# Performance work log

Measured on AMD Instinct MI355X. Metric: run time of the kernel, lower is better.

The kernel has to match this reference:

```python
import jax, jax.numpy as jnp
import numpy as np

B, NQ, NKV, D, H, HD = 8, 1024, 2048, 1024, 16, 64  # inner_dim = H*HD = 1024


def setup_inputs() -> dict:
    key = jax.random.key(0)
    ks = jax.random.split(key, 10)
    s = 0.02
    return {
        "latent": jax.random.normal(ks[0], (B, NQ, D), jnp.float32),
        "data": jax.random.normal(ks[1], (B, NKV, D), jnp.float32),
        "wq": jax.random.normal(ks[2], (D, H * HD), jnp.float32) * s,
        "bq": jax.random.normal(ks[3], (H * HD,), jnp.float32) * s,
        "wk": jax.random.normal(ks[4], (D, H * HD), jnp.float32) * s,
        "bk": jax.random.normal(ks[5], (H * HD,), jnp.float32) * s,
        "wv": jax.random.normal(ks[6], (D, H * HD), jnp.float32) * s,
        "bv": jax.random.normal(ks[7], (H * HD,), jnp.float32) * s,
        "wo": jax.random.normal(ks[8], (H * HD, D), jnp.float32) * s,
        "bo": jax.random.normal(ks[9], (D,), jnp.float32) * s,
    }


def reference(latent, data, wq, bq, wk, bk, wv, bv, wo, bo):
    scale = HD ** -0.5
    # projections: [b, n, H*HD] -> [b, h, n, d]
    def split_heads(t):
        b, n, _ = t.shape
        return t.reshape(b, n, H, HD).transpose(0, 2, 1, 3)

    q = split_heads(latent @ wq + bq)   # [b, h, nq, d]
    k = split_heads(data @ wk + bk)     # [b, h, nkv, d]
    v = split_heads(data @ wv + bv)     # [b, h, nkv, d]

    scores = jnp.einsum("bhid,bhjd->bhij", q, k) * scale  # [b, h, nq, nkv]
    att = jax.nn.softmax(scores, axis=-1)                  # dropout p=0 (eval)
    out = jnp.einsum("bhij,bhjd->bhid", att, v)            # [b, h, nq, d]
    out = out.transpose(0, 2, 1, 3).reshape(B, NQ, H * HD)
    return out @ wo + bo
```

## Files before the change

### kernel.cpp

```cpp
#include <hip/hip_runtime.h>
#include <hip/hip_bf16.h>
#include <math.h>


using short8  = __attribute__((ext_vector_type(8))) short;
using f32x4   = __attribute__((ext_vector_type(4))) float;
using uint4v  = __attribute__((ext_vector_type(4))) unsigned int;

__device__ __forceinline__ ushort f2bf(float f) {
    unsigned u = __builtin_bit_cast(unsigned, f);
    u = (u + 0x7FFFu + ((u >> 16) & 1u)) >> 16;
    return (ushort)u;
}
__device__ __forceinline__ unsigned pack_bf2(float lo, float hi) {
    unsigned ulo = __builtin_bit_cast(unsigned, lo) + 0x8000u;
    unsigned uhi = __builtin_bit_cast(unsigned, hi) + 0x8000u;
    return __builtin_amdgcn_perm(uhi, ulo, 0x07060302);
}

__device__ __forceinline__ void gld_lds16(const ushort* g, ushort* l) {
    __builtin_amdgcn_global_load_lds(
        (const __attribute__((address_space(1))) unsigned int*)(const void*)g,
        (__attribute__((address_space(3))) unsigned int*)(void*)l,
        16, 0, 0);
}

__global__ void prep_fused(const float* __restrict__ latent, const float* __restrict__ data,
                           const float* __restrict__ wq, const float* __restrict__ wk,
                           const float* __restrict__ wv, const float* __restrict__ wo,
                           ushort* __restrict__ latB, ushort* __restrict__ datB,
                           ushort* __restrict__ wqT, ushort* __restrict__ wkT,
                           ushort* __restrict__ wvT, ushort* __restrict__ woT) {
    __shared__ ushort tile[32][33];
    const int bx  = blockIdx.x;
    const int tid = threadIdx.x;
    if (bx < 12288) {
        const float* in = (bx < 4096) ? latent : data;
        ushort* out     = (bx < 4096) ? latB : datB;
        int idx = (bx < 4096) ? bx : bx - 4096;
        int i = (idx * 256 + tid) * 8;
        float4 a = *(const float4*)(in + i);
        float4 b = *(const float4*)(in + i + 4);
        short8 o;
        o[0] = (short)f2bf(a.x); o[1] = (short)f2bf(a.y);
        o[2] = (short)f2bf(a.z); o[3] = (short)f2bf(a.w);
        o[4] = (short)f2bf(b.x); o[5] = (short)f2bf(b.y);
        o[6] = (short)f2bf(b.z); o[7] = (short)f2bf(b.w);
        *(short8*)(out + i) = o;
        return;
    }
    int rem = bx - 12288;
    int z   = rem >> 10;
    int bxx = rem & 31;
    int byy = (rem >> 5) & 31;
    const float* in = (z == 0) ? wq : (z == 1) ? wk : (z == 2) ? wv : wo;
    ushort* out     = (z == 0) ? wqT : (z == 1) ? wkT : (z == 2) ? wvT : woT;
    int tx = tid & 31, ty = tid >> 5;
    int x = bxx * 32 + tx;
    int y = byy * 32;
#pragma unroll
    for (int i = 0; i < 32; i += 8)
        tile[ty + i][tx] = f2bf(in[(size_t)(y + ty + i) * 1024 + x]);
    __syncthreads();
    int x2 = byy * 32 + tx;
    int y2 = bxx * 32;
#pragma unroll
    for (int i = 0; i < 32; i += 8)
        out[(size_t)(y2 + ty + i) * 1024 + x2] = tile[tx][ty + i];
}

template <int S>
__device__ __forceinline__ void stage_half(const ushort* __restrict__ G, int rbase,
                                           ushort* tile, int H, int kcol,
                                           int wave, int lane) {
#pragma unroll
    for (int c = 0; c < 2; ++c) {
        int rho = c * 64 + wave * 8;
        int gr0 = (rho / S) * (2 * S) + H * S + (rho % S);
        int rig = lane >> 3;
        int q   = (lane & 7) ^ rig;
        gld_lds16(G + (size_t)(rbase + gr0 + rig) * 1024 + kcol + q * 8,
                  tile + gr0 * 64);
    }
}

__device__ __forceinline__ void gemm256_body(
        const ushort* __restrict__ A, const ushort* __restrict__ Bt,
        const float* __restrict__ bias, void* __restrict__ Cv,
        float scale, int mode, int bm, int bn) {
    __shared__ __align__(16) ushort sm[65536];
    ushort* As0 = sm;
    ushort* Bs0 = sm + 16384;
    ushort* As1 = sm + 32768;
    ushort* Bs1 = sm + 49152;

    const int tid  = threadIdx.x;
    const int wave = tid >> 6, lane = tid & 63;
    const int l15 = lane & 15, quad = lane >> 4;
    const int wm = wave >> 2, wn = wave & 3;
    const int m0 = bm * 256, n0 = bn * 256;

    const int rA  = wm * 128 + l15;
    const int rB  = wn * 64 + l15;
    const int cq0 = quad ^ (l15 & 7);
    const int cq1 = (4 + quad) ^ (l15 & 7);

    stage_half<64>(A,  m0, As0, 0, 0,  wave, lane);
    stage_half<32>(Bt, n0, Bs0, 0, 0,  wave, lane);
    stage_half<32>(Bt, n0, Bs0, 1, 0,  wave, lane);
    stage_half<64>(A,  m0, As0, 1, 0,  wave, lane);
    stage_half<64>(A,  m0, As1, 0, 64, wave, lane);
    stage_half<32>(Bt, n0, Bs1, 1, 64, wave, lane);
    stage_half<64>(A,  m0, As1, 1, 64, wave, lane);
    asm volatile("s_waitcnt vmcnt(6)" ::: "memory");
    __builtin_amdgcn_s_barrier();

    f32x4 acc[8][4] = {};

#define LDA(MH)                                                                   \
    _Pragma("unroll")                                                             \
    for (int mi = 0; mi < 4; ++mi) {                                              \
        a[mi][0] = *(const short8*)(Ac + (rA + (MH) * 64 + mi * 16) * 64 + cq0 * 8); \
        a[mi][1] = *(const short8*)(Ac + (rA + (MH) * 64 + mi * 16) * 64 + cq1 * 8); \
    }
#define LDB(NH)                                                                   \
    _Pragma("unroll")                                                             \
    for (int ni = 0; ni < 2; ++ni) {                                              \
        b[ni][0] = *(const short8*)(Bc + (rB + (NH) * 32 + ni * 16) * 64 + cq0 * 8); \
        b[ni][1] = *(const short8*)(Bc + (rB + (NH) * 32 + ni * 16) * 64 + cq1 * 8); \
    }
#define MFMA_PHASE(MB, NB)                                                        \
    __builtin_amdgcn_s_barrier();                                                 \
    asm volatile("s_waitcnt lgkmcnt(0)" ::: "memory");                            \
    __builtin_amdgcn_sched_barrier(0);                                            \
    __builtin_amdgcn_s_setprio(1);                                                \
    _Pragma("unroll")                                                             \
    for (int mi = 0; mi < 4; ++mi)                                                \
        _Pragma("unroll")                                                         \
        for (int ni = 0; ni < 2; ++ni)                                            \
            _Pragma("unroll")                                                     \
            for (int kk = 0; kk < 2; ++kk)                                        \
                acc[(MB) * 4 + mi][(NB) * 2 + ni] =                               \
                    __builtin_amdgcn_mfma_f32_16x16x32_bf16(                      \
                        a[mi][kk], b[ni][kk], acc[(MB) * 4 + mi][(NB) * 2 + ni],  \
                        0, 0, 0);                                                 \
    __builtin_amdgcn_s_setprio(0);                                                \
    __builtin_amdgcn_s_barrier();

#pragma unroll 2
    for (int g = 0; g < 16; ++g) {
        ushort* Ac = (g & 1) ? As1 : As0;
        ushort* Bc = (g & 1) ? Bs1 : Bs0;
        ushort* Bn = (g & 1) ? Bs0 : Bs1;
        const int k1 = ((g + 1) & 15) * 64;
        const int k2 = ((g + 2) & 15) * 64;
        short8 a[4][2], b[2][2];

        LDA(0) LDB(0)
        stage_half<32>(Bt, n0, Bn, 0, k1, wave, lane);
        MFMA_PHASE(0, 0)

        LDB(1)
        stage_half<64>(A, m0, Ac, 0, k2, wave, lane);
        MFMA_PHASE(0, 1)

        LDA(1)
        stage_half<32>(Bt, n0, Bc, 1, k2, wave, lane);
        MFMA_PHASE(1, 1)

        LDB(0)
        stage_half<64>(A, m0, Ac, 1, k2, wave, lane);
        asm volatile("s_waitcnt vmcnt(6)" ::: "memory");
        MFMA_PHASE(1, 0)
    }
#undef LDA
#undef LDB
#undef MFMA_PHASE

    asm volatile("s_waitcnt vmcnt(0)" ::: "memory");

    float bvv[4];
    int   cols[4];
#pragma unroll
    for (int n4 = 0; n4 < 4; ++n4) {
        cols[n4] = n0 + wn * 64 + n4 * 16 + l15;
        bvv[n4]  = bias[cols[n4]];
    }
#pragma unroll
    for (int m8 = 0; m8 < 8; ++m8) {
        int rbase = m0 + wm * 128 + m8 * 16 + quad * 4;
#pragma unroll
        for (int n4 = 0; n4 < 4; ++n4) {
            float v[4];
#pragma unroll
            for (int rr = 0; rr < 4; ++rr)
                v[rr] = (acc[m8][n4][rr] + bvv[n4]) * scale;
            if (mode == 1) {
                int kvl = rbase & 2047;
                int pos = (kvl & ~31) + ((kvl >> 2) & 3) * 8 + ((kvl >> 4) & 1) * 4;
                size_t base = ((size_t)((rbase >> 11) * 1024 + cols[n4])) * 2048 + pos;
                uint2 o;
                o.x = pack_bf2(v[0], v[1]);
                o.y = pack_bf2(v[2], v[3]);
                *(uint2*)((ushort*)Cv + base) = o;
            } else if (mode == 0) {
#pragma unroll
                for (int rr = 0; rr < 4; ++rr)
                    ((ushort*)Cv)[(size_t)(rbase + rr) * 1024 + cols[n4]] = f2bf(v[rr]);
            } else {
#pragma unroll
                for (int rr = 0; rr < 4; ++rr)
                    ((float*)Cv)[(size_t)(rbase + rr) * 1024 + cols[n4]] = v[rr];
            }
        }
    }
}

__global__ __launch_bounds__(512, 2) void proj_qkv(
        const ushort* __restrict__ latB, const ushort* __restrict__ datB,
        const ushort* __restrict__ wqT, const ushort* __restrict__ wkT,
        const ushort* __restrict__ wvT,
        const float* __restrict__ bq, const float* __restrict__ bk,
        const float* __restrict__ bv,
        ushort* __restrict__ Qb, ushort* __restrict__ Kb, ushort* __restrict__ Vtb,
        float qscale) {
    int bid = ((int)blockIdx.x & 7) * 80 + ((int)blockIdx.x >> 3);
    const ushort* A;
    const ushort* W;
    const float*  bias;
    void*         C;
    float sc;
    int mode, idx;
    if (bid < 128)      { A = latB; W = wqT; bias = bq; C = Qb;  sc = qscale; mode = 0; idx = bid; }
    else if (bid < 384) { A = datB; W = wkT; bias = bk; C = Kb;  sc = 1.f;    mode = 0; idx = bid - 128; }
    else                { A = datB; W = wvT; bias = bv; C = Vtb; sc = 1.f;    mode = 1; idx = bid - 384; }
    gemm256_body(A, W, bias, C, sc, mode, idx >> 2, idx & 3);
}

template <int MODE>
__global__ void gemm_bt(const ushort* __restrict__ A, const ushort* __restrict__ Bt,
                        const float* __restrict__ bias, void* __restrict__ Cv,
                        int K, float scale) {
    __shared__ __align__(16) ushort As[128 * 32];
    __shared__ __align__(16) ushort Bs[128 * 32];
    const int tid  = threadIdx.x;
    const int wave = tid >> 6, lane = tid & 63;
    const int l15 = lane & 15, quad = lane >> 4;
    const int wm = wave & 1, wn = wave >> 1;
    const int m0 = blockIdx.x * 128;
    const int n0 = blockIdx.y * 128;

    f32x4 acc[4][4] = {};

    for (int k0 = 0; k0 < K; k0 += 32) {
        __syncthreads();
#pragma unroll
        for (int i = 0; i < 2; ++i) {
            int f   = (i * 256 + tid) * 8;
            int row = f >> 5, col = f & 31;
            gld_lds16(A  + (size_t)(m0 + row) * K + k0 + col, As + (i * 256 + wave * 64) * 8);
            gld_lds16(Bt + (size_t)(n0 + row) * K + k0 + col, Bs + (i * 256 + wave * 64) * 8);
        }
        __syncthreads();

        short8 a[4], b[4];
#pragma unroll
        for (int mi = 0; mi < 4; ++mi)
            a[mi] = *(const short8*)(As + (wm * 64 + mi * 16 + l15) * 32 + quad * 8);
#pragma unroll
        for (int ni = 0; ni < 4; ++ni)
            b[ni] = *(const short8*)(Bs + (wn * 64 + ni * 16 + l15) * 32 + quad * 8);
#pragma unroll
        for (int mi = 0; mi < 4; ++mi)
#pragma unroll
            for (int ni = 0; ni < 4; ++ni)
                acc[mi][ni] = __builtin_amdgcn_mfma_f32_16x16x32_bf16(a[mi], b[ni], acc[mi][ni], 0, 0, 0);
    }

    float bv[4];
    int   cols[4];
#pragma unroll
    for (int ni = 0; ni < 4; ++ni) {
        cols[ni] = n0 + wn * 64 + ni * 16 + l15;
        bv[ni]   = bias[cols[ni]];
    }
#pragma unroll
    for (int mi = 0; mi < 4; ++mi) {
        int rbase = m0 + wm * 64 + mi * 16 + quad * 4;
#pragma unroll
        for (int ni = 0; ni < 4; ++ni) {
            float v[4];
#pragma unroll
            for (int rr = 0; rr < 4; ++rr)
                v[rr] = (acc[mi][ni][rr] + bv[ni]) * scale;
            if (MODE == 1) {
                int kvl = rbase & 2047;
                int pos = (kvl & ~31) + ((kvl >> 2) & 3) * 8 + ((kvl >> 4) & 1) * 4;
                size_t base = ((size_t)((rbase >> 11) * 1024 + cols[ni])) * 2048 + pos;
                uint2 o;
                o.x = pack_bf2(v[0], v[1]);
                o.y = pack_bf2(v[2], v[3]);
                *(uint2*)((ushort*)Cv + base) = o;
            } else {
#pragma unroll
                for (int rr = 0; rr < 4; ++rr) {
                    int row = rbase + rr;
                    if (MODE == 0)
                        ((ushort*)Cv)[(size_t)row * 1024 + cols[ni]] = f2bf(v[rr]);
                    else
                        ((float*)Cv)[(size_t)row * 1024 + cols[ni]] = v[rr];
                }
            }
        }
    }
}

__global__ __launch_bounds__(256, 3) void attn_fused(const ushort* __restrict__ Q,
                                                     const ushort* __restrict__ K,
                                                     const ushort* __restrict__ Vt,
                                                     ushort* __restrict__ O) {
    __shared__ __align__(16) ushort smem[2 * 8192];
    ushort* Ks  = smem;
    ushort* Vts = smem + 8192;

    const int tid  = threadIdx.x;
    const int wave = tid >> 6, lane = tid & 63;
    const int l15 = lane & 15, quad = lane >> 4;
    const int bx = blockIdx.x;
    const int bh = bx & 127, h = bh & 15, b = bh >> 4;
    const int q0 = (bx >> 7) * 128;

    const ushort* Qg = Q + ((size_t)(b * 1024 + q0)) * 1024 + h * 64;
    const ushort* Kg = K + ((size_t)(b * 2048)) * 1024 + h * 64;
    const ushort* Vg = Vt + ((size_t)(b * 1024 + h * 64)) * 2048;

    short8 bq[2][2];
#pragma unroll
    for (int qt = 0; qt < 2; ++qt) {
        int row = wave * 32 + qt * 16 + l15;
#pragma unroll
        for (int ks = 0; ks < 2; ++ks)
            bq[ks][qt] = *(const short8*)(Qg + (size_t)row * 1024 + ks * 32 + quad * 8);
    }

    f32x4 Oacc[4][2] = {};
    float l_run[2] = {0.f, 0.f};

    const int rig = lane >> 3;
    const int scb8 = (lane & 7) ^ rig;
    const int riv = lane >> 4;
    const int cb16 = lane & 15;

    short8 kreg[4], vreg[4];
#pragma unroll
    for (int g = 0; g < 4; ++g) {
        int G = wave * 4 + g;
        kreg[g] = *(const short8*)(Kg + (size_t)(G * 8 + rig) * 1024 + scb8 * 8);
        int vrow = G * 4 + riv;
        int scv = cb16 ^ (vrow & 15);
        vreg[g] = *(const short8*)(Vg + (size_t)vrow * 2048 + scv * 8);
    }

    for (int kv0 = 0; kv0 < 2048; kv0 += 128) {
        __syncthreads();
#pragma unroll
        for (int g = 0; g < 4; ++g) {
            int G = wave * 4 + g;
            *(short8*)(Ks  + G * 512 + lane * 8) = kreg[g];
            *(short8*)(Vts + G * 512 + lane * 8) = vreg[g];
        }
        __syncthreads();

        if (kv0 + 128 < 2048) {
            int kvn = kv0 + 128;
#pragma unroll
            for (int g = 0; g < 4; ++g) {
                int G = wave * 4 + g;
                kreg[g] = *(const short8*)(Kg + (size_t)(kvn + G * 8 + rig) * 1024 + scb8 * 8);
                int vrow = G * 4 + riv;
                int scv = cb16 ^ (vrow & 15);
                vreg[g] = *(const short8*)(Vg + (size_t)vrow * 2048 + kvn + scv * 8);
            }
        }

        unsigned pk[8][2][2];
#pragma unroll
        for (int kvt = 0; kvt < 8; ++kvt) {
            f32x4 s0 = {}, s1 = {};
#pragma unroll
            for (int ks = 0; ks < 2; ++ks) {
                int ck = ((ks * 4 + quad) ^ (l15 & 7)) * 8;
                short8 ak = *(const short8*)(Ks + (kvt * 16 + l15) * 64 + ck);
                s0 = __builtin_amdgcn_mfma_f32_16x16x32_bf16(ak, bq[ks][0], s0, 0, 0, 0);
                s1 = __builtin_amdgcn_mfma_f32_16x16x32_bf16(ak, bq[ks][1], s1, 0, 0, 0);
            }
            float p0[4], p1[4];
#pragma unroll
            for (int rr = 0; rr < 4; ++rr) {
                p0[rr] = __builtin_amdgcn_exp2f(s0[rr]);
                p1[rr] = __builtin_amdgcn_exp2f(s1[rr]);
                l_run[0] += p0[rr];
                l_run[1] += p1[rr];
            }
            pk[kvt][0][0] = pack_bf2(p0[0], p0[1]);
            pk[kvt][0][1] = pack_bf2(p0[2], p0[3]);
            pk[kvt][1][0] = pack_bf2(p1[0], p1[1]);
            pk[kvt][1][1] = pack_bf2(p1[2], p1[3]);
        }

#pragma unroll
        for (int sp = 0; sp < 4; ++sp) {
#pragma unroll
            for (int dt = 0; dt < 4; ++dt) {
                int cv = ((sp * 4 + quad) ^ l15) * 8;
                short8 av = *(const short8*)(Vts + (dt * 16 + l15) * 128 + cv);
#pragma unroll
                for (int qt = 0; qt < 2; ++qt) {
                    uint4v u = {pk[2 * sp][qt][0], pk[2 * sp][qt][1],
                                pk[2 * sp + 1][qt][0], pk[2 * sp + 1][qt][1]};
                    short8 bp = __builtin_bit_cast(short8, u);
                    Oacc[dt][qt] = __builtin_amdgcn_mfma_f32_16x16x32_bf16(av, bp, Oacc[dt][qt], 0, 0, 0);
                }
            }
        }
    }

#pragma unroll
    for (int qt = 0; qt < 2; ++qt) {
        float l = l_run[qt];
        l += __shfl_xor(l, 16);
        l += __shfl_xor(l, 32);
        float inv = 1.f / l;
        int qg = q0 + wave * 32 + qt * 16 + l15;
#pragma unroll
        for (int dt = 0; dt < 4; ++dt) {
            uint2 o;
            o.x = pack_bf2(Oacc[dt][qt][0] * inv, Oacc[dt][qt][1] * inv);
            o.y = pack_bf2(Oacc[dt][qt][2] * inv, Oacc[dt][qt][3] * inv);
            *(uint2*)(O + ((size_t)(b * 1024 + qg)) * 1024 + h * 64 + dt * 16 + quad * 4) = o;
        }
    }
}

extern "C" void kernel_launch(void* const* d_in, const int* in_sizes, int n_in,
                              void* d_out, int out_size, void* d_ws, size_t ws_size,
                              hipStream_t stream) {
    const float* latent = (const float*)d_in[0];
    const float* data   = (const float*)d_in[1];
    const float* wq     = (const float*)d_in[2];
    const float* bq     = (const float*)d_in[3];
    const float* wk     = (const float*)d_in[4];
    const float* bk     = (const float*)d_in[5];
    const float* wv     = (const float*)d_in[6];
    const float* bv     = (const float*)d_in[7];
    const float* wo     = (const float*)d_in[8];
    const float* bo     = (const float*)d_in[9];
    float* out = (float*)d_out;

    ushort* ws   = (ushort*)d_ws;
    ushort* wqT  = ws;
    ushort* wkT  = wqT + (1u << 20);
    ushort* wvT  = wkT + (1u << 20);
    ushort* woT  = wvT + (1u << 20);
    ushort* latB = woT + (1u << 20);
    ushort* datB = latB + (8u << 20);
    ushort* Qb   = datB + (16u << 20);
    ushort* Kb   = Qb + (8u << 20);
    ushort* Vtb  = Kb + (16u << 20);
    ushort* AO   = latB;

    prep_fused<<<dim3(16384), 256, 0, stream>>>(latent, data, wq, wk, wv, wo,
                                                latB, datB, wqT, wkT, wvT, woT);

    const float qscale = 0.125f * 1.44269504088896340736f;
    proj_qkv<<<dim3(640), 512, 0, stream>>>(latB, datB, wqT, wkT, wvT,
                                            bq, bk, bv, Qb, Kb, Vtb, qscale);
    attn_fused<<<dim3(1024), 256, 0, stream>>>(Qb, Kb, Vtb, AO);
    gemm_bt<2><<<dim3(64, 8), 256, 0, stream>>>(AO, woT, bo, out, 1024, 1.0f);
}
```

Baseline: 371.6 us.

## Load attention K/V tiles directly into LDS, raise occupancy, batch GEMM B-fragment loads

In the attention kernel, the register-staged prefetch of K and V^T is replaced by direct global-to-LDS loads issued at the start of each KV tile. The kernel targets 4 waves per SIMD instead of 3 and raises wave priority during the MFMA/softmax section. Freeing the prefetch registers is meant to buy occupancy, but loads are no longer overlapped with compute inside a block, so the added waves must hide that latency instead. In the projection GEMM, all four B fragments are read from LDS once per k-step instead of being reloaded in three phases, which cuts LDS reads at the cost of more live registers.

```diff
diff --git a/kernel.cpp b/kernel.cpp
--- a/kernel.cpp
+++ b/kernel.cpp
@@ -123,11 +123,11 @@
         a[mi][0] = *(const short8*)(Ac + (rA + (MH) * 64 + mi * 16) * 64 + cq0 * 8); \
         a[mi][1] = *(const short8*)(Ac + (rA + (MH) * 64 + mi * 16) * 64 + cq1 * 8); \
     }
-#define LDB(NH)                                                                   \
+#define LDB_ALL                                                                   \
     _Pragma("unroll")                                                             \
-    for (int ni = 0; ni < 2; ++ni) {                                              \
-        b[ni][0] = *(const short8*)(Bc + (rB + (NH) * 32 + ni * 16) * 64 + cq0 * 8); \
-        b[ni][1] = *(const short8*)(Bc + (rB + (NH) * 32 + ni * 16) * 64 + cq1 * 8); \
+    for (int nj = 0; nj < 4; ++nj) {                                              \
+        b[nj][0] = *(const short8*)(Bc + (rB + nj * 16) * 64 + cq0 * 8);          \
+        b[nj][1] = *(const short8*)(Bc + (rB + nj * 16) * 64 + cq1 * 8);          \
     }
 #define MFMA_PHASE(MB, NB)                                                        \
     __builtin_amdgcn_s_barrier();                                                 \
@@ -142,8 +142,8 @@
             for (int kk = 0; kk < 2; ++kk)                                        \
                 acc[(MB) * 4 + mi][(NB) * 2 + ni] =                               \
                     __builtin_amdgcn_mfma_f32_16x16x32_bf16(                      \
-                        a[mi][kk], b[ni][kk], acc[(MB) * 4 + mi][(NB) * 2 + ni],  \
-                        0, 0, 0);                                                 \
+                        a[mi][kk], b[(NB) * 2 + ni][kk],                          \
+                        acc[(MB) * 4 + mi][(NB) * 2 + ni], 0, 0, 0);              \
     __builtin_amdgcn_s_setprio(0);                                                \
     __builtin_amdgcn_s_barrier();
 
@@ -154,13 +154,12 @@
         ushort* Bn = (g & 1) ? Bs0 : Bs1;
         const int k1 = ((g + 1) & 15) * 64;
         const int k2 = ((g + 2) & 15) * 64;
-        short8 a[4][2], b[2][2];
-
-        LDA(0) LDB(0)
+        short8 a[4][2], b[4][2];
+
+        LDA(0) LDB_ALL
         stage_half<32>(Bt, n0, Bn, 0, k1, wave, lane);
         MFMA_PHASE(0, 0)
 
-        LDB(1)
         stage_half<64>(A, m0, Ac, 0, k2, wave, lane);
         MFMA_PHASE(0, 1)
 
@@ -168,13 +167,12 @@
         stage_half<32>(Bt, n0, Bc, 1, k2, wave, lane);
         MFMA_PHASE(1, 1)
 
-        LDB(0)
         stage_half<64>(A, m0, Ac, 1, k2, wave, lane);
         asm volatile("s_waitcnt vmcnt(6)" ::: "memory");
         MFMA_PHASE(1, 0)
     }
 #undef LDA
-#undef LDB
+#undef LDB_ALL
 #undef MFMA_PHASE
 
     asm volatile("s_waitcnt vmcnt(0)" ::: "memory");
@@ -315,7 +313,7 @@
     }
 }
 
-__global__ __launch_bounds__(256, 3) void attn_fused(const ushort* __restrict__ Q,
+__global__ __launch_bounds__(256, 4) void attn_fused(const ushort* __restrict__ Q,
                                                      const ushort* __restrict__ K,
                                                      const ushort* __restrict__ Vt,
                                                      ushort* __restrict__ O) {
@@ -351,38 +349,19 @@
     const int riv = lane >> 4;
     const int cb16 = lane & 15;
 
-    short8 kreg[4], vreg[4];
-#pragma unroll
-    for (int g = 0; g < 4; ++g) {
-        int G = wave * 4 + g;
-        kreg[g] = *(const short8*)(Kg + (size_t)(G * 8 + rig) * 1024 + scb8 * 8);
-        int vrow = G * 4 + riv;
-        int scv = cb16 ^ (vrow & 15);
-        vreg[g] = *(const short8*)(Vg + (size_t)vrow * 2048 + scv * 8);
-    }
-
     for (int kv0 = 0; kv0 < 2048; kv0 += 128) {
         __syncthreads();
 #pragma unroll
         for (int g = 0; g < 4; ++g) {
             int G = wave * 4 + g;
-            *(short8*)(Ks  + G * 512 + lane * 8) = kreg[g];
-            *(short8*)(Vts + G * 512 + lane * 8) = vreg[g];
+            gld_lds16(Kg + (size_t)(kv0 + G * 8 + rig) * 1024 + scb8 * 8, Ks + G * 512);
+            int vrow = G * 4 + riv;
+            int scv = cb16 ^ (vrow & 15);
+            gld_lds16(Vg + (size_t)vrow * 2048 + kv0 + scv * 8, Vts + G * 512);
         }
         __syncthreads();
 
-        if (kv0 + 128 < 2048) {
-            int kvn = kv0 + 128;
-#pragma unroll
-            for (int g = 0; g < 4; ++g) {
-                int G = wave * 4 + g;
-                kreg[g] = *(const short8*)(Kg + (size_t)(kvn + G * 8 + rig) * 1024 + scb8 * 8);
-                int vrow = G * 4 + riv;
-                int scv = cb16 ^ (vrow & 15);
-                vreg[g] = *(const short8*)(Vg + (size_t)vrow * 2048 + kvn + scv * 8);
-            }
-        }
-
+        __builtin_amdgcn_s_setprio(1);
         unsigned pk[8][2][2];
 #pragma unroll
         for (int kvt = 0; kvt < 8; ++kvt) {
@@ -423,6 +402,7 @@
                 }
             }
         }
+        __builtin_amdgcn_s_setprio(0);
     }
 
 #pragma unroll
```

Result: no change. 364.5 us (-1.9%).
